# Optimization experiments

Hardware: AMD Instinct MI355X
Metric: run time of the kernel (lower is better)

Reference implementation:

```python
import jax, jax.numpy as jnp
import numpy as np

HIDDEN = 2560
NUM_HEADS = 80
HEAD_DIM = 64
STATE = 128
N_GROUPS = 1
CONV_K = 4
CHUNK = 256
INTER = 2 * HIDDEN                       # 5120 = NUM_HEADS * HEAD_DIM
CONV_DIM = INTER + 2 * N_GROUPS * STATE  # 5376
PROJ = INTER + CONV_DIM + NUM_HEADS      # 10576
EPS = 1e-5
DT_MIN, DT_MAX = 0.0, 100.0


def segment_sum(x):
    # x: (..., T) -> (..., T, T); out[i, j] = sum_{j < k <= i} x[k], -inf above diag
    T = x.shape[-1]
    xe = jnp.broadcast_to(x[..., :, None], x.shape + (T,))  # [i, j] = x[i]
    mask_lo = jnp.tril(jnp.ones((T, T), dtype=bool), -1)
    seg = jnp.cumsum(jnp.where(mask_lo, xe, 0.0), axis=-2)
    mask = jnp.tril(jnp.ones((T, T), dtype=bool), 0)
    return jnp.where(mask, seg, -jnp.inf)


def setup_inputs() -> dict:
    key = jax.random.key(0)
    k0, k1, k2, k3 = jax.random.split(key, 4)
    x = jax.random.normal(k0, (2, 2048, HIDDEN), jnp.float32)
    in_proj_w = jax.random.normal(k1, (PROJ, HIDDEN), jnp.float32) * (HIDDEN ** -0.5)
    conv1d_w = jax.random.normal(k2, (CONV_DIM, CONV_K), jnp.float32) * (CONV_K ** -0.5)
    conv1d_b = jnp.zeros((CONV_DIM,), jnp.float32)
    A_log = jnp.log(jnp.arange(1, NUM_HEADS + 1, dtype=jnp.float32))
    D = jnp.ones((NUM_HEADS,), jnp.float32)
    dt_bias = jnp.ones((NUM_HEADS,), jnp.float32)
    norm_weight = jnp.ones((INTER,), jnp.float32)
    out_proj_w = jax.random.normal(k3, (HIDDEN, INTER), jnp.float32) * (INTER ** -0.5)
    return dict(input_states=x, in_proj_w=in_proj_w, conv1d_w=conv1d_w,
                conv1d_b=conv1d_b, A_log=A_log, D=D, dt_bias=dt_bias,
                norm_weight=norm_weight, out_proj_w=out_proj_w)


def _mamba2_forward(input_states, in_proj_w, conv1d_w, conv1d_b, A_log, D,
                    dt_bias, norm_weight, out_proj_w):
    b, s, _ = input_states.shape
    proj = input_states @ in_proj_w.T                       # (b, s, PROJ)
    gate, hs, dt = jnp.split(proj, [INTER, INTER + CONV_DIM], axis=-1)

    # causal depthwise conv1d + SiLU
    xT = jnp.transpose(hs, (0, 2, 1))                       # (b, conv_dim, s)
    xT = jnp.pad(xT, ((0, 0), (0, 0), (CONV_K - 1, 0)))
    conv = jax.lax.conv_general_dilated(
        xT, conv1d_w[:, None, :], (1,), 'VALID',
        feature_group_count=CONV_DIM, dimension_numbers=('NCH', 'OIH', 'NCH'))
    hs = jax.nn.silu(jnp.transpose(conv + conv1d_b[None, :, None], (0, 2, 1)))

    hs, B, C = jnp.split(hs, [INTER, INTER + N_GROUPS * STATE], axis=-1)
    A = -jnp.exp(A_log)                                     # (h,)
    dt = jnp.clip(jax.nn.softplus(dt + dt_bias), DT_MIN, DT_MAX)  # (b, s, h)

    X = hs.reshape(b, s, NUM_HEADS, HEAD_DIM)
    rep = NUM_HEADS // N_GROUPS
    B = jnp.repeat(B.reshape(b, s, N_GROUPS, STATE), rep, axis=2)
    C = jnp.repeat(C.reshape(b, s, N_GROUPS, STATE), rep, axis=2)

    pad = (-s) % CHUNK
    D_res = D[None, None, :, None] * jnp.pad(X, ((0, 0), (0, pad), (0, 0), (0, 0)))
    Xd = X * dt[..., None]                                  # discretized input
    dA = A[None, None, :] * dt                              # (b, s, h)

    def chunk(t):
        t = jnp.pad(t, [(0, 0), (0, pad)] + [(0, 0)] * (t.ndim - 2))
        return t.reshape(t.shape[0], -1, CHUNK, *t.shape[2:])

    Xc, Bc, Cc = chunk(Xd), chunk(B), chunk(C)              # (b, c, l, h, ...)
    Ac = jnp.transpose(chunk(dA), (0, 3, 1, 2))             # (b, h, c, l)
    A_cum = jnp.cumsum(Ac, axis=-1)

    # 1. intra-chunk (diagonal block) outputs
    L = jnp.exp(segment_sum(Ac))                            # (b, h, c, l, l)
    G = jnp.einsum('bclhn,bcshn->bhcls', Cc, Bc)
    Y_diag = jnp.einsum('bhcls,bcshp->bclhp', G * L, Xc)

    # 2. per-chunk final states
    decay_states = jnp.exp(A_cum[..., -1:] - A_cum)         # (b, h, c, l)
    states = jnp.einsum('bclhn,bhcl,bclhp->bchpn', Bc, decay_states, Xc)

    # 3. inter-chunk recurrence
    A_last = A_cum[..., -1]                                 # (b, h, c)
    decay_chunk = jnp.exp(segment_sum(jnp.pad(A_last, ((0, 0), (0, 0), (1, 0)))))
    states = jnp.concatenate([jnp.zeros_like(states[:, :1]), states], axis=1)
    new_states = jnp.einsum('bhzc,bchpn->bzhpn', decay_chunk, states)
    states = new_states[:, :-1]                             # (b, c, h, p, n)

    # 4. state -> output conversion
    Y_off = jnp.einsum('bclhn,bchpn,bhcl->bclhp', Cc, states, jnp.exp(A_cum))

    y = (Y_diag + Y_off).reshape(b, -1, NUM_HEADS, HEAD_DIM) + D_res
    y = y[:, :s].reshape(b, s, INTER)

    # gated RMSNorm
    y = y * jax.nn.silu(gate)
    var = jnp.mean(y * y, axis=-1, keepdims=True)
    y = y * jax.lax.rsqrt(var + EPS) * norm_weight
    return y @ out_proj_w.T


def reference(input_states, in_proj_w, conv1d_w, conv1d_b, A_log, D, dt_bias,
              norm_weight, out_proj_w):
    return _mamba2_forward(input_states, in_proj_w, conv1d_w, conv1d_b, A_log,
                           D, dt_bias, norm_weight, out_proj_w)
```

## Files before the change

kernel.cpp:

```cpp
#include <hip/hip_runtime.h>
#include <hip/hip_bf16.h>
#include <math.h>

#define HIDDEN   2560
#define NUM_HEADS 80
#define HEAD_DIM 64
#define STATE    128
#define CONV_K   4
#define CHUNK    256
#define INTER    (2*HIDDEN)
#define CONV_DIM (INTER + 2*STATE)
#define PROJ     (INTER + CONV_DIM + NUM_HEADS)
#define PROJ_PAD 10240
#define NBC      336
#define NBCP     384
#define EPS      1e-5f

#define BATCH 2
#define SEQ   2048
#define TOK   (BATCH*SEQ)
#define NC    (SEQ/CHUNK)
#define KSPL2 8
#define KCH2  (HIDDEN/KSPL2)

#define RED_BLOCKS 1536
#define CXT_BLOCKS 5120
#define CBC_BLOCKS 4096
#define CUM_BLOCKS 1280
#define W2_BLOCKS  12800
#define ST_BLOCKS  1280
#define GK_BLOCKS  576

typedef __attribute__((ext_vector_type(8))) short bf16x8;
typedef __attribute__((ext_vector_type(4))) float f32x4;
typedef unsigned short us;

#define MFMA16(a,b,c) __builtin_amdgcn_mfma_f32_16x16x32_bf16((a),(b),(c),0,0,0)

__device__ __forceinline__ us f2bf(float f){
    union{float f;unsigned u;}v; v.f=f;
    unsigned r = v.u + 0x7fffu + ((v.u>>16)&1u);
    return (us)(r>>16);
}
__device__ __forceinline__ float bf2f(us s){
    union{unsigned u;float f;}v; v.u = ((unsigned)s)<<16; return v.f;
}
__device__ __forceinline__ void unpack8(uint4 u, float* e){
    e[0]=bf2f((us)(u.x&0xffff)); e[1]=bf2f((us)(u.x>>16));
    e[2]=bf2f((us)(u.y&0xffff)); e[3]=bf2f((us)(u.y>>16));
    e[4]=bf2f((us)(u.z&0xffff)); e[5]=bf2f((us)(u.z>>16));
    e[6]=bf2f((us)(u.w&0xffff)); e[7]=bf2f((us)(u.w>>16));
}
__device__ __forceinline__ void gld16(const void* g, void* l){
    __builtin_amdgcn_global_load_lds((const __attribute__((address_space(1))) void*)g,
                                     (__attribute__((address_space(3))) void*)l, 16, 0, 0);
}

template<bool BF16OUT>
__global__ __launch_bounds__(256) void gemm_bf16(const us* __restrict__ A, int lda,
                                                 const us* __restrict__ B, int ldb,
                                                 void* __restrict__ Cv, int ldc, int K) {
    __shared__ us As[128][64];
    __shared__ us Bs[128][64];
    int tid = threadIdx.x;
    int lane = tid & 63, wid = tid >> 6;
    int wr = wid >> 1, wc = wid & 1;

    int bm, bn;
    if ((gridDim.y & 7) == 0) {
        int bid   = blockIdx.y * gridDim.x + blockIdx.x;
        int xcd   = bid & 7;
        int local = bid >> 3;
        int mrows = gridDim.y >> 3;
        bm = (xcd * mrows + (local % mrows)) * 128;
        bn = (local / mrows) * 128;
    } else {
        bm = blockIdx.y * 128;
        bn = blockIdx.x * 128;
    }

    f32x4 acc[4][4];
    #pragma unroll
    for (int i=0;i<4;i++)
        #pragma unroll
        for (int j=0;j<4;j++) acc[i][j] = (f32x4){0.f,0.f,0.f,0.f};

    int srow_off = lane >> 3;
    int sslot    = lane & 7;

    for (int k0 = 0; k0 < K; k0 += 64) {
        #pragma unroll
        for (int q=0;q<4;q++){
            int brow = (wid*4+q)*8;
            int row  = brow + srow_off;
            int sl   = sslot ^ (row & 7);
            gld16(A + (size_t)(bm + row)*lda + k0 + sl*8, &As[brow][0]);
            gld16(B + (size_t)(bn + row)*ldb + k0 + sl*8, &Bs[brow][0]);
        }
        __syncthreads();
        #pragma unroll
        for (int kk=0; kk<64; kk+=32){
            bf16x8 a[4], b[4];
            #pragma unroll
            for (int i=0;i<4;i++){
                int row = wr*64 + i*16 + (lane&15);
                int slot = ((kk>>3) + (lane>>4)) ^ (row & 7);
                a[i] = *(const bf16x8*)&As[row][slot*8];
            }
            #pragma unroll
            for (int j=0;j<4;j++){
                int row = wc*64 + j*16 + (lane&15);
                int slot = ((kk>>3) + (lane>>4)) ^ (row & 7);
                b[j] = *(const bf16x8*)&Bs[row][slot*8];
            }
            #pragma unroll
            for (int i=0;i<4;i++)
                #pragma unroll
                for (int j=0;j<4;j++)
                    acc[i][j] = MFMA16(a[i], b[j], acc[i][j]);
        }
        __syncthreads();
    }
    #pragma unroll
    for (int i=0;i<4;i++){
        int row0 = bm + wr*64 + i*16 + (lane>>4)*4;
        #pragma unroll
        for (int j=0;j<4;j++){
            int col = bn + wc*64 + j*16 + (lane&15);
            #pragma unroll
            for (int r=0;r<4;r++){
                if (BF16OUT)
                    ((us*)Cv)[(size_t)(row0+r)*ldc + col] = f2bf(acc[i][j][r]);
                else
                    ((float*)Cv)[(size_t)(row0+r)*ldc + col] = acc[i][j][r];
            }
        }
    }
}

__global__ __launch_bounds__(256) void bc_splitk_mfma(const us* __restrict__ xhi,
                                                      const us* __restrict__ xlo,
                                                      const us* __restrict__ whi,
                                                      const us* __restrict__ wlo,
                                                      float* __restrict__ Cpart) {
    __shared__ us As[128][64];
    __shared__ us Bs[128][64];
    int tid = threadIdx.x;
    int lane = tid & 63, wid = tid >> 6;
    int wr = wid >> 1, wc = wid & 1;
    int bn = blockIdx.x * 128, bm = blockIdx.y * 128, z = blockIdx.z;

    f32x4 acc[4][4];
    #pragma unroll
    for (int i=0;i<4;i++)
        #pragma unroll
        for (int j=0;j<4;j++) acc[i][j] = (f32x4){0.f,0.f,0.f,0.f};

    int srow_off = lane >> 3;
    int sslot    = lane & 7;

    for (int term = 0; term < 3; ++term){
        const us* A = (term==2) ? xlo : xhi;
        const us* B = (term==0) ? wlo : whi;
        for (int k0 = z*KCH2; k0 < z*KCH2 + KCH2; k0 += 64) {
            #pragma unroll
            for (int q=0;q<4;q++){
                int brow = (wid*4+q)*8;
                int row  = brow + srow_off;
                int sl   = sslot ^ (row & 7);
                gld16(A + (size_t)(bm + row)*HIDDEN + k0 + sl*8, &As[brow][0]);
                gld16(B + (size_t)(bn + row)*HIDDEN + k0 + sl*8, &Bs[brow][0]);
            }
            __syncthreads();
            #pragma unroll
            for (int kk=0; kk<64; kk+=32){
                bf16x8 a[4], b[4];
                #pragma unroll
                for (int i=0;i<4;i++){
                    int row = wr*64 + i*16 + (lane&15);
                    int slot = ((kk>>3) + (lane>>4)) ^ (row & 7);
                    a[i] = *(const bf16x8*)&As[row][slot*8];
                }
                #pragma unroll
                for (int j=0;j<4;j++){
                    int row = wc*64 + j*16 + (lane&15);
                    int slot = ((kk>>3) + (lane>>4)) ^ (row & 7);
                    b[j] = *(const bf16x8*)&Bs[row][slot*8];
                }
                #pragma unroll
                for (int i=0;i<4;i++)
                    #pragma unroll
                    for (int j=0;j<4;j++)
                        acc[i][j] = MFMA16(a[i], b[j], acc[i][j]);
            }
            __syncthreads();
        }
    }
    float* Cz = Cpart + (size_t)z*TOK*NBCP;
    #pragma unroll
    for (int i=0;i<4;i++){
        int row0 = bm + wr*64 + i*16 + (lane>>4)*4;
        #pragma unroll
        for (int j=0;j<4;j++){
            int col = bn + wc*64 + j*16 + (lane&15);
            #pragma unroll
            for (int r=0;r<4;r++)
                Cz[(size_t)(row0+r)*NBCP + col] = acc[i][j][r];
        }
    }
}

#define N4A ((size_t)TOK*HIDDEN/4)
#define N4B ((size_t)PROJ_PAD*HIDDEN/4)
#define N4C ((size_t)NBCP*HIDDEN/4)
__global__ __launch_bounds__(256) void prep_kernel(const float* __restrict__ x,
                                                   const float* __restrict__ in_w,
                                                   us* __restrict__ xhi,
                                                   us* __restrict__ xlo,
                                                   us* __restrict__ w1b,
                                                   us* __restrict__ wbc_hi,
                                                   us* __restrict__ wbc_lo) {
    size_t gid = (size_t)blockIdx.x*256 + threadIdx.x;
    if (gid < N4A) {
        size_t i = gid*4;
        float4 v = *(const float4*)(x + i);
        float e[4] = {v.x, v.y, v.z, v.w};
        ushort4 h, l;
        us* hp = (us*)&h;
        us* lp = (us*)&l;
        #pragma unroll
        for (int u=0;u<4;u++){
            us hv = f2bf(e[u]);
            hp[u] = hv;
            lp[u] = f2bf(e[u] - bf2f(hv));
        }
        *(ushort4*)(xhi + i) = h;
        *(ushort4*)(xlo + i) = l;
    } else if (gid < N4A + N4B) {
        size_t i = (gid - N4A)*4;
        float4 v = *(const float4*)(in_w + i);
        ushort4 o;
        o.x=f2bf(v.x); o.y=f2bf(v.y); o.z=f2bf(v.z); o.w=f2bf(v.w);
        *(ushort4*)(w1b + i) = o;
    } else {
        size_t j = gid - N4A - N4B;
        size_t i = j*4;
        int row = (int)(i / HIDDEN);
        int kk  = (int)(i % HIDDEN);
        ushort4 h, l;
        h.x=h.y=h.z=h.w=0; l.x=l.y=l.z=l.w=0;
        if (row < NBC){
            float4 v = *(const float4*)(in_w + (size_t)(2*INTER + row)*HIDDEN + kk);
            float e[4] = {v.x, v.y, v.z, v.w};
            us* hp = (us*)&h;
            us* lp = (us*)&l;
            #pragma unroll
            for (int u=0;u<4;u++){
                us hv = f2bf(e[u]);
                hp[u] = hv;
                lp[u] = f2bf(e[u] - bf2f(hv));
            }
        }
        *(ushort4*)(wbc_hi + i) = h;
        *(ushort4*)(wbc_lo + i) = l;
    }
}

__global__ __launch_bounds__(256) void mega_red_convxt(const float* __restrict__ part,
                                                       const float* __restrict__ dt_bias,
                                                       const us* __restrict__ projb,
                                                       const float* __restrict__ cw,
                                                       const float* __restrict__ cb,
                                                       float* __restrict__ outBC,
                                                       float* __restrict__ dtbuf,
                                                       us* __restrict__ XT) {
    __shared__ us raw[68][66];
    int bid = blockIdx.x;
    int tid = threadIdx.x;
    if (bid < RED_BLOCKS) {
        size_t i4 = (size_t)bid*256 + tid;
        size_t i = i4*4;
        float4 s = *(const float4*)(part + i);
        #pragma unroll
        for (int z=1; z<KSPL2; z++){
            float4 v = *(const float4*)(part + (size_t)z*TOK*NBCP + i);
            s.x += v.x; s.y += v.y; s.z += v.z; s.w += v.w;
        }
        int col = (int)(i % NBCP);
        int t   = (int)(i / NBCP);
        if (col < 256) {
            *(float4*)(outBC + (size_t)t*NBC + col) = s;
        } else if (col < NBC) {
            int h = col - 256;
            float e[4] = {s.x, s.y, s.z, s.w};
            #pragma unroll
            for (int u=0;u<4;u++){
                float xv = e[u] + dt_bias[h+u];
                float sp = (xv > 20.f) ? xv : log1pf(expf(xv));
                e[u] = fminf(fmaxf(sp, 0.f), 100.f);
            }
            float4 o; o.x=e[0]; o.y=e[1]; o.z=e[2]; o.w=e[3];
            *(float4*)(dtbuf + (size_t)t*NUM_HEADS + h) = o;
        }
    } else {
        int b3 = bid - RED_BLOCKS;
        int bx = b3 & 63, by = b3 >> 6;
        int t0 = bx * 64, d0 = by * 64;
        int b  = t0 / SEQ;
        int s0 = t0 % SEQ;
        for (int f = tid; f < 67*8; f += 256){
            int r = f >> 3, g = f & 7;
            int sp = s0 - 3 + r;
            uint4 v;
            if (sp >= 0) v = *(const uint4*)(projb + ((size_t)(b*SEQ+sp))*PROJ_PAD + INTER + d0 + g*8);
            else { v.x=0u; v.y=0u; v.z=0u; v.w=0u; }
            unsigned int* dst = (unsigned int*)&raw[r][g*8];
            dst[0]=v.x; dst[1]=v.y; dst[2]=v.z; dst[3]=v.w;
        }
        __syncthreads();
        int t = tid & 63, dg = tid >> 6;
        #pragma unroll
        for (int dd = 0; dd < 16; dd++){
            int d = dg*16 + dd;
            float acc = cb[d0+d];
            #pragma unroll
            for (int j=0;j<CONV_K;j++)
                acc += cw[(d0+d)*CONV_K+j] * bf2f(raw[t+j][d]);
            float val = acc/(1.f+expf(-acc));
            XT[((size_t)(b*INTER + d0 + d))*SEQ + s0 + t] = f2bf(val);
        }
    }
}

__global__ __launch_bounds__(256) void mega_convbc_cum_w2(const float* __restrict__ projBC,
                                                          const float* __restrict__ cw,
                                                          const float* __restrict__ cb,
                                                          const float* __restrict__ dtbuf,
                                                          const float* __restrict__ A_log,
                                                          const float* __restrict__ out_w,
                                                          float* __restrict__ xBC_BC,
                                                          us* __restrict__ BT,
                                                          us* __restrict__ Cb,
                                                          float* __restrict__ A_cum,
                                                          us* __restrict__ w2b) {
    __shared__ float buf[CHUNK];
    int bid = blockIdx.x;
    int tid = threadIdx.x;
    if (bid < CBC_BLOCKS) {
        int idx = bid*256 + tid;
        int d = idx & 255;
        int t = idx >> 8;
        int b = t / SEQ, sl = t % SEQ;
        int dc = INTER + d;
        float acc = cb[dc];
        #pragma unroll
        for (int j=0;j<CONV_K;j++){
            int sp = sl - (CONV_K-1) + j;
            if (sp >= 0)
                acc += cw[dc*CONV_K+j] * projBC[((size_t)(b*SEQ+sp))*NBC + d];
        }
        float val = acc / (1.f + expf(-acc));
        xBC_BC[(size_t)t*256 + d] = val;
        if (d < 128)
            BT[((size_t)(b*128 + d))*SEQ + sl] = f2bf(val);
        else
            Cb[(size_t)t*128 + (d-128)] = f2bf(val);
    } else if (bid < CBC_BLOCKS + CUM_BLOCKS) {
        int b4 = bid - CBC_BLOCKS;
        int c = b4 & 7, h = (b4 >> 3) % 80, b = b4 / 640;
        int l = tid;
        float A = -expf(A_log[h]);
        float v = A * dtbuf[(size_t)(b*SEQ + c*CHUNK + l)*NUM_HEADS + h];
        buf[l] = v;
        __syncthreads();
        for (int off=1; off<CHUNK; off<<=1){
            float t2 = (l>=off) ? buf[l-off] : 0.f;
            __syncthreads();
            buf[l] += t2;
            __syncthreads();
        }
        A_cum[((size_t)b*NUM_HEADS + h)*SEQ + c*CHUNK + l] = buf[l];
    } else {
        size_t i4 = (size_t)(bid - CBC_BLOCKS - CUM_BLOCKS)*256 + tid;
        size_t i = i4*4;
        float4 v = *(const float4*)(out_w + i);
        ushort4 o; o.x=f2bf(v.x); o.y=f2bf(v.y); o.z=f2bf(v.z); o.w=f2bf(v.w);
        *(ushort4*)(w2b + i) = o;
    }
}

__global__ __launch_bounds__(256) void mega_states_g(const us* __restrict__ XT,
                                                     const us* __restrict__ BT,
                                                     const float* __restrict__ dtbuf,
                                                     const float* __restrict__ A_cum,
                                                     const float* __restrict__ xBC_BC,
                                                     us* __restrict__ statesT,
                                                     us* __restrict__ G) {
    __shared__ __align__(16) char SH[33792];
    int bid = blockIdx.x;
    int tid = threadIdx.x;
    if (bid < ST_BLOCKS) {
        int c = bid & 7, h = (bid >> 3) % 80, b = bid / 640;
        us (*Asx)[64] = (us(*)[64])SH;
        us (*Bs)[64]  = (us(*)[64])(SH + 8192);
        float* wl     = (float*)(SH + 24576);
        int lane = tid & 63, wid = tid >> 6;
        {
            const float* ac = A_cum + ((size_t)(b*NUM_HEADS+h))*SEQ + c*CHUNK;
            float Alast = ac[CHUNK-1];
            wl[tid] = expf(Alast - ac[tid]) * dtbuf[((size_t)(b*SEQ + c*CHUNK + tid))*NUM_HEADS + h];
        }
        __syncthreads();
        f32x4 acc[4][2];
        #pragma unroll
        for (int i=0;i<4;i++)
            #pragma unroll
            for (int j=0;j<2;j++) acc[i][j] = (f32x4){0.f,0.f,0.f,0.f};

        for (int kc = 0; kc < 4; kc++){
            int lbase = kc*64;
            #pragma unroll
            for (int q=0;q<4;q++){
                int brow = (wid*4+q)*8;
                int row  = brow + (lane>>3);
                int sl   = (lane&7) ^ (row & 7);
                gld16(BT + ((size_t)(b*128 + row))*SEQ + c*CHUNK + lbase + sl*8, &Bs[brow][0]);
            }
            #pragma unroll
            for (int it=0; it<2; it++){
                int f = tid + it*256;
                int r = f >> 3, g = f & 7;
                uint4 v = *(const uint4*)(XT + ((size_t)(b*INTER + h*HEAD_DIM + r))*SEQ + c*CHUNK + lbase + g*8);
                float e[8]; unpack8(v, e);
                us o[8];
                #pragma unroll
                for (int u=0;u<8;u++) o[u] = f2bf(e[u] * wl[lbase + g*8 + u]);
                int slot = g ^ (r & 7);
                *(ushort4*)&Asx[r][slot*8]   = *(ushort4*)&o[0];
                *(ushort4*)&Asx[r][slot*8+4] = *(ushort4*)&o[4];
            }
            __syncthreads();
            #pragma unroll
            for (int kk=0; kk<64; kk+=32){
                bf16x8 a[4], bb[2];
                #pragma unroll
                for (int i=0;i<4;i++){
                    int row = i*16 + (lane&15);
                    int slot = ((kk>>3)+(lane>>4)) ^ (row&7);
                    a[i] = *(const bf16x8*)&Asx[row][slot*8];
                }
                #pragma unroll
                for (int j=0;j<2;j++){
                    int row = wid*32 + j*16 + (lane&15);
                    int slot = ((kk>>3)+(lane>>4)) ^ (row&7);
                    bb[j] = *(const bf16x8*)&Bs[row][slot*8];
                }
                #pragma unroll
                for (int i=0;i<4;i++)
                    #pragma unroll
                    for (int j=0;j<2;j++)
                        acc[i][j] = MFMA16(a[i], bb[j], acc[i][j]);
            }
            __syncthreads();
        }
        size_t sb = ((size_t)((b*NC + c)*NUM_HEADS + h))*(HEAD_DIM*STATE);
        #pragma unroll
        for (int i=0;i<4;i++){
            #pragma unroll
            for (int j=0;j<2;j++){
                int n = wid*32 + j*16 + (lane&15);
                int p0 = i*16 + (lane>>4)*4;
                #pragma unroll
                for (int r=0;r<4;r++)
                    statesT[sb + (size_t)(p0+r)*128 + n] = f2bf(acc[i][j][r]);
            }
        }
    } else {
        int b5 = bid - ST_BLOCKS;
        int c = b5 & 7, p = (b5 >> 3) % 36, b = b5 / 288;
        int lt = 0, a0 = 0;
        while (a0 + lt + 1 <= p) { a0 += lt + 1; lt++; }
        int st = p - a0;
        int l0 = lt*32, s0 = st*32;
        float (*Cs)[132] = (float(*)[132])SH;
        float (*Bs2)[132] = (float(*)[132])(SH + 16896);
        int ty = tid >> 4, tx = tid & 15;
        float acc[2][2];
        acc[0][0]=0.f; acc[0][1]=0.f; acc[1][0]=0.f; acc[1][1]=0.f;

        size_t rowC = ((size_t)(b*SEQ + c*CHUNK + l0))*256 + 128;
        size_t rowB = ((size_t)(b*SEQ + c*CHUNK + s0))*256;
        #pragma unroll
        for (int it=0; it<4; it++){
            int f = tid + it*256;
            int r = f >> 5, c4 = f & 31;
            *(float4*)&Cs[r][c4*4]  = *(const float4*)(xBC_BC + rowC + (size_t)r*256 + c4*4);
            *(float4*)&Bs2[r][c4*4] = *(const float4*)(xBC_BC + rowB + (size_t)r*256 + c4*4);
        }
        __syncthreads();
        #pragma unroll 8
        for (int k=0;k<128;k++){
            float a0v = Cs[ty*2][k],   a1v = Cs[ty*2+1][k];
            float b0v = Bs2[tx*2][k],  b1v = Bs2[tx*2+1][k];
            acc[0][0] += a0v*b0v; acc[0][1] += a0v*b1v;
            acc[1][0] += a1v*b0v; acc[1][1] += a1v*b1v;
        }
        size_t Gb = ((size_t)(b*NC + c)) << 16;
        #pragma unroll
        for (int i=0;i<2;i++){
            ushort2 g2;
            g2.x = f2bf(acc[i][0]); g2.y = f2bf(acc[i][1]);
            *(ushort2*)(G + Gb + (size_t)(l0 + ty*2 + i)*256 + s0 + tx*2) = g2;
        }
    }
}

__global__ __launch_bounds__(256) void recur_kernel(const float* __restrict__ A_cum,
                                                    us* __restrict__ states) {
    int h = blockIdx.x, b = blockIdx.y, z = blockIdx.z;
    int tid = threadIdx.x;
    float Srun[8];
    #pragma unroll
    for (int i=0;i<8;i++) Srun[i]=0.f;
    const float* acum = A_cum + ((size_t)b*NUM_HEADS + h)*SEQ;
    for (int c=0;c<NC;c++){
        float alast = acum[c*CHUNK + CHUNK-1];
        float dec = expf(alast);
        size_t base = ((size_t)((b*NC + c)*NUM_HEADS + h))*(HEAD_DIM*STATE);
        #pragma unroll
        for (int i=0;i<8;i++){
            size_t idx = base + (size_t)tid + (size_t)(z*8+i)*256;
            float raw = bf2f(states[idx]);
            states[idx] = f2bf(Srun[i]);
            Srun[i] = Srun[i]*dec + raw;
        }
    }
}

__global__ __launch_bounds__(256) void yscan_mfma(const us* __restrict__ G,
                                                  const us* __restrict__ Cb,
                                                  const us* __restrict__ XT,
                                                  const float* __restrict__ dtbuf,
                                                  const float* __restrict__ A_cum,
                                                  const us* __restrict__ statesT,
                                                  const float* __restrict__ Dvec,
                                                  us* __restrict__ projb) {
    int xb = blockIdx.x;
    int c = xb & 7, lt = xb >> 3;
    int h = blockIdx.y, b = blockIdx.z;
    int l0 = lt*64;
    __shared__ __align__(16) char pool[32768];
    us (*Cs)[128] = (us(*)[128])pool;
    us (*St)[128] = (us(*)[128])(pool + 16384);
    us (*Gw)[64]  = (us(*)[64])pool;
    us (*Xs)[64]  = (us(*)[64])(pool + 8192);
    float (*Ot)[68] = (float(*)[68])pool;
    __shared__ float ac[CHUNK], dts[CHUNK];
    int tid = threadIdx.x, lane = tid & 63, wid = tid >> 6;
    ac[tid]  = A_cum[((size_t)(b*NUM_HEADS + h))*SEQ + c*CHUNK + tid];
    dts[tid] = dtbuf[((size_t)(b*SEQ + c*CHUNK + tid))*NUM_HEADS + h];

    size_t stb = ((size_t)((b*NC + c)*NUM_HEADS + h))*(HEAD_DIM*STATE);
    #pragma unroll
    for (int q=0;q<4;q++){
        int brow = (wid*4+q)*4;
        int row  = brow + (lane>>4);
        int sl   = (lane&15) ^ (row & 7);
        gld16(Cb + ((size_t)(b*SEQ + c*CHUNK + l0 + row))*128 + sl*8, &Cs[brow][0]);
        gld16(statesT + stb + (size_t)row*128 + sl*8, &St[brow][0]);
    }
    __syncthreads();

    f32x4 acc1[4];
    #pragma unroll
    for (int j=0;j<4;j++) acc1[j] = (f32x4){0.f,0.f,0.f,0.f};
    #pragma unroll
    for (int kk=0; kk<128; kk+=32){
        int arow = wid*16 + (lane&15);
        int aslot = ((kk>>3)+(lane>>4)) ^ (arow&7);
        bf16x8 a = *(const bf16x8*)&Cs[arow][aslot*8];
        #pragma unroll
        for (int j=0;j<4;j++){
            int brow = j*16 + (lane&15);
            int bslot = ((kk>>3)+(lane>>4)) ^ (brow&7);
            bf16x8 bb = *(const bf16x8*)&St[brow][bslot*8];
            acc1[j] = MFMA16(a, bb, acc1[j]);
        }
    }
    float el[4];
    #pragma unroll
    for (int r=0;r<4;r++) el[r] = expf(ac[l0 + wid*16 + (lane>>4)*4 + r]);
    float master[4][4];
    #pragma unroll
    for (int j=0;j<4;j++)
        #pragma unroll
        for (int r=0;r<4;r++) master[j][r] = acc1[j][r]*el[r];
    __syncthreads();

    size_t Gb = ((size_t)(b*NC + c)) << 16;
    f32x4 acc2[4];
    #pragma unroll
    for (int j=0;j<4;j++) acc2[j] = (f32x4){0.f,0.f,0.f,0.f};
    for (int st=0; st<=lt; st++){
        int s0 = st*64;
        #pragma unroll
        for (int it=0; it<2; it++){
            int f = tid + it*256;
            int r = f >> 3, g = f & 7;
            uint4 v = *(const uint4*)(G + Gb + (size_t)(l0 + r)*256 + s0 + g*8);
            float e[8]; unpack8(v, e);
            float acl = ac[l0 + r];
            us o[8];
            #pragma unroll
            for (int u=0;u<8;u++){
                int s = s0 + g*8 + u;
                float w = (s <= l0 + r) ? expf(acl - ac[s])*dts[s] : 0.f;
                o[u] = f2bf(e[u]*w);
            }
            int slot = g ^ (r&7);
            *(ushort4*)&Gw[r][slot*8]   = *(ushort4*)&o[0];
            *(ushort4*)&Gw[r][slot*8+4] = *(ushort4*)&o[4];
        }
        #pragma unroll
        for (int q=0;q<2;q++){
            int brow = (wid*2+q)*8;
            int row  = brow + (lane>>3);
            int sl   = (lane&7) ^ (row&7);
            gld16(XT + ((size_t)(b*INTER + h*HEAD_DIM + row))*SEQ + c*CHUNK + s0 + sl*8,
                  &Xs[brow][0]);
        }
        __syncthreads();
        #pragma unroll
        for (int kk=0; kk<64; kk+=32){
            int arow = wid*16 + (lane&15);
            int aslot = ((kk>>3)+(lane>>4)) ^ (arow&7);
            bf16x8 a = *(const bf16x8*)&Gw[arow][aslot*8];
            #pragma unroll
            for (int j=0;j<4;j++){
                int brow = j*16 + (lane&15);
                int bslot = ((kk>>3)+(lane>>4)) ^ (brow&7);
                bf16x8 bb = *(const bf16x8*)&Xs[brow][bslot*8];
                acc2[j] = MFMA16(a, bb, acc2[j]);
            }
        }
        if (st < lt) __syncthreads();
    }

    float Dh = Dvec[h];
    #pragma unroll
    for (int j=0;j<4;j++){
        int p = j*16 + (lane&15);
        #pragma unroll
        for (int r=0;r<4;r++){
            int sl_ = wid*16 + (lane>>4)*4 + r;
            int slot = (sl_>>3) ^ (p&7);
            float xv = bf2f(Xs[p][slot*8 + (sl_&7)]);
            master[j][r] += acc2[j][r] + Dh*xv;
        }
    }
    __syncthreads();

    #pragma unroll
    for (int j=0;j<4;j++){
        int p = j*16 + (lane&15);
        #pragma unroll
        for (int r=0;r<4;r++)
            Ot[wid*16 + (lane>>4)*4 + r][p] = master[j][r];
    }
    __syncthreads();
    #pragma unroll
    for (int it=0; it<4; it++){
        int f = tid + it*256;
        int r = f >> 4, c4 = f & 15;
        ushort4 o;
        o.x = f2bf(Ot[r][c4*4+0]); o.y = f2bf(Ot[r][c4*4+1]);
        o.z = f2bf(Ot[r][c4*4+2]); o.w = f2bf(Ot[r][c4*4+3]);
        *(ushort4*)(projb + ((size_t)(b*SEQ + c*CHUNK + l0 + r))*PROJ_PAD + INTER + h*HEAD_DIM + c4*4) = o;
    }
}

__global__ __launch_bounds__(256) void gate_norm_kernel(const us* __restrict__ projb,
                                                        const float* __restrict__ normw,
                                                        us* __restrict__ yb) {
    int t = blockIdx.x;
    int tid = threadIdx.x;
    const us* row = projb + (size_t)t*PROJ_PAD;
    __shared__ float red[4];
    float vals[20];
    float ss = 0.f;
    #pragma unroll
    for (int i=0;i<5;i++){
        int j = (tid + i*256)*4;
        ushort4 g4 = *(const ushort4*)(row + j);
        ushort4 y4 = *(const ushort4*)(row + INTER + j);
        #pragma unroll
        for (int u=0;u<4;u++){
            float g = bf2f(((const us*)&g4)[u]);
            float y = bf2f(((const us*)&y4)[u]);
            float gv = g / (1.f + expf(-g));
            float v = y * gv;
            vals[i*4+u] = v;
            ss += v*v;
        }
    }
    #pragma unroll
    for (int off=32; off; off>>=1) ss += __shfl_xor(ss, off);
    if ((tid&63)==0) red[tid>>6] = ss;
    __syncthreads();
    float tot = red[0]+red[1]+red[2]+red[3];
    float inv = rsqrtf(tot/(float)INTER + EPS);
    #pragma unroll
    for (int i=0;i<5;i++){
        int j = (tid + i*256)*4;
        ushort4 o;
        o.x = f2bf(vals[i*4+0] * inv * normw[j+0]);
        o.y = f2bf(vals[i*4+1] * inv * normw[j+1]);
        o.z = f2bf(vals[i*4+2] * inv * normw[j+2]);
        o.w = f2bf(vals[i*4+3] * inv * normw[j+3]);
        *(ushort4*)(yb + (size_t)t*INTER + j) = o;
    }
}

extern "C" void kernel_launch(void* const* d_in, const int* in_sizes, int n_in,
                              void* d_out, int out_size, void* d_ws, size_t ws_size,
                              hipStream_t stream) {
    const float* x        = (const float*)d_in[0];
    const float* in_w     = (const float*)d_in[1];
    const float* conv_w   = (const float*)d_in[2];
    const float* conv_b   = (const float*)d_in[3];
    const float* A_log    = (const float*)d_in[4];
    const float* Dvec     = (const float*)d_in[5];
    const float* dt_bias  = (const float*)d_in[6];
    const float* norm_w   = (const float*)d_in[7];
    const float* out_w    = (const float*)d_in[8];
    float* out = (float*)d_out;
    (void)ws_size; (void)n_in; (void)in_sizes; (void)out_size;

    const size_t PROJB   = (size_t)TOK*PROJ_PAD*2;
    const size_t PROJBCB = (size_t)TOK*NBC*4;
    const size_t XTB     = (size_t)TOK*INTER*2;
    const size_t XBCBCB  = (size_t)TOK*256*4;
    const size_t BTB     = (size_t)BATCH*128*SEQ*2;
    const size_t CBB     = (size_t)TOK*128*2;
    const size_t GBYTES  = (size_t)BATCH*NC*CHUNK*CHUNK*2;
    const size_t DTB     = (size_t)TOK*NUM_HEADS*4;
    const size_t ACUMB   = DTB;
    const size_t STB     = (size_t)BATCH*NC*NUM_HEADS*HEAD_DIM*STATE*2;
    const size_t XHB   = (size_t)TOK*HIDDEN*2;
    const size_t WBCB  = (size_t)NBCP*HIDDEN*2;
    const size_t YBB   = (size_t)TOK*INTER*2;

    char* base = (char*)d_ws;
    size_t off = 0;
    us* projb  = (us*)(base + off); off += PROJB;
    float* projBC = (float*)(base + off); off += PROJBCB;
    us* XTp    = (us*)(base + off); off += XTB;
    float* xBC_BC = (float*)(base + off); off += XBCBCB;
    us* BTp    = (us*)(base + off); off += BTB;
    us* Cbp    = (us*)(base + off); off += CBB;
    us* Gp     = (us*)(base + off); off += GBYTES;
    float* dtbuf = (float*)(base + off); off += DTB;
    float* A_cum = (float*)(base + off); off += ACUMB;
    us* statesT = (us*)(base + off); off += STB;
    char*  T   = base + off;
    us* xhi    = (us*)T;
    us* xlo    = (us*)(T + XHB);
    us* wbc_hi = (us*)(T + 2*XHB);
    us* wbc_lo = (us*)(T + 2*XHB + WBCB);
    us* w1b    = (us*)(T + 2*XHB + 2*WBCB);
    float* bcpart = (float*)w1b;
    us* yb     = (us*)T;
    us* w2b    = (us*)(T + YBB);

    {
        unsigned total_blocks = (unsigned)((N4A + N4B + N4C) / 256);
        prep_kernel<<<total_blocks, 256, 0, stream>>>(x, in_w, xhi, xlo, w1b, wbc_hi, wbc_lo);
    }
    gemm_bf16<true><<<dim3(PROJ_PAD/128, TOK/128), 256, 0, stream>>>(xhi, HIDDEN, w1b, HIDDEN,
                                                                     projb, PROJ_PAD, HIDDEN);
    bc_splitk_mfma<<<dim3(NBCP/128, TOK/128, KSPL2), 256, 0, stream>>>(xhi, xlo, wbc_hi, wbc_lo, bcpart);
    mega_red_convxt<<<RED_BLOCKS + CXT_BLOCKS, 256, 0, stream>>>(bcpart, dt_bias, projb,
                                                                 conv_w, conv_b,
                                                                 projBC, dtbuf, XTp);
    mega_convbc_cum_w2<<<CBC_BLOCKS + CUM_BLOCKS + W2_BLOCKS, 256, 0, stream>>>(
        projBC, conv_w, conv_b, dtbuf, A_log, out_w, xBC_BC, BTp, Cbp, A_cum, w2b);
    mega_states_g<<<ST_BLOCKS + GK_BLOCKS, 256, 0, stream>>>(XTp, BTp, dtbuf, A_cum, xBC_BC,
                                                             statesT, Gp);
    recur_kernel<<<dim3(NUM_HEADS, BATCH, 4), 256, 0, stream>>>(A_cum, statesT);
    yscan_mfma<<<dim3(NC*4, NUM_HEADS, BATCH), 256, 0, stream>>>(Gp, Cbp, XTp, dtbuf, A_cum,
                                                                 statesT, Dvec, projb);
    gate_norm_kernel<<<TOK, 256, 0, stream>>>(projb, norm_w, yb);
    gemm_bf16<false><<<dim3(HIDDEN/128, TOK/128), 256, 0, stream>>>(yb, INTER, w2b, INTER,
                                                                    out, HIDDEN, INTER);
}
```

Baseline: 705.1 us.

## Replace input projection GEMM with 256x256 tile, 8-wave phased pipelined kernel

Swaps the 128x128-tile input projection GEMM for a new 512-thread kernel that computes 256x256 output tiles. It double-buffers K-halves in LDS through direct global-to-LDS loads and interleaves prefetch stages with MFMA sub-phases under explicit waitcnt and barrier control, raising s_setprio around the MFMA bursts. The larger tile raises arithmetic intensity and the phased schedule aims to hide load latency. In exchange it uses more registers per thread and gives a smaller grid (40x16 blocks), which may reduce occupancy and leave tail imbalance.

```diff
diff --git a/kernel.cpp b/kernel.cpp
--- a/kernel.cpp
+++ b/kernel.cpp
@@ -54,6 +54,99 @@
 __device__ __forceinline__ void gld16(const void* g, void* l){
     __builtin_amdgcn_global_load_lds((const __attribute__((address_space(1))) void*)g,
                                      (__attribute__((address_space(3))) void*)l, 16, 0, 0);
+}
+
+__global__ __launch_bounds__(512) void gemm1_8ph(const us* __restrict__ A,
+                                                 const us* __restrict__ B,
+                                                 us* __restrict__ C, int ldc) {
+    __shared__ us LA[2][2][256][32];
+    __shared__ us LB[2][2][256][32];
+    int tid = threadIdx.x, lane = tid & 63, wid = tid >> 6;
+    int wm = wid >> 2, wn = wid & 3;
+
+    int bid   = blockIdx.y * gridDim.x + blockIdx.x;
+    int xcd   = bid & 7;
+    int local = bid >> 3;
+    int mrows = gridDim.y >> 3;
+    int bm = (xcd * mrows + (local % mrows)) * 256;
+    int bn = (local / mrows) * 256;
+
+    f32x4 acc[8][4];
+    #pragma unroll
+    for (int i=0;i<8;i++)
+        #pragma unroll
+        for (int j=0;j<4;j++) acc[i][j] = (f32x4){0.f,0.f,0.f,0.f};
+
+    const int NT = HIDDEN/64;
+
+    #define STGA(TT,KH) { _Pragma("unroll")                                        \
+        for (int q=0;q<2;q++){                                                     \
+            int brow=(wid*2+q)*16; int row=brow+(lane>>2);                         \
+            int sl=(lane&3)^((row>>1)&3);                                          \
+            gld16(A + (size_t)(bm+row)*HIDDEN + (TT)*64 + (KH)*32 + sl*8,          \
+                  &LA[(TT)&1][KH][brow][0]); } }
+    #define STGB(TT,KH) { _Pragma("unroll")                                        \
+        for (int q=0;q<2;q++){                                                     \
+            int brow=(wid*2+q)*16; int row=brow+(lane>>2);                         \
+            int sl=(lane&3)^((row>>1)&3);                                          \
+            gld16(B + (size_t)(bn+row)*HIDDEN + (TT)*64 + (KH)*32 + sl*8,          \
+                  &LB[(TT)&1][KH][brow][0]); } }
+
+    STGA(0,0); STGB(0,0); STGA(0,1); STGB(0,1); STGA(1,0); STGB(1,0);
+    asm volatile("s_waitcnt vmcnt(8)" ::: "memory");
+    asm volatile("s_barrier" ::: "memory");
+
+    for (int t = 0; t < NT; ++t) {
+        int par = t & 1;
+        #pragma unroll
+        for (int sub = 0; sub < 4; ++sub) {
+            const int kh = sub >> 1, mg = sub & 1;
+            bf16x8 afr[4], bfr[4];
+            #pragma unroll
+            for (int mi=0;mi<4;mi++){
+                int row = wm*128 + (mg*4+mi)*16 + (lane&15);
+                int sl  = (lane>>4) ^ ((row>>1)&3);
+                afr[mi] = *(const bf16x8*)&LA[par][kh][row][sl*8];
+            }
+            #pragma unroll
+            for (int nj=0;nj<4;nj++){
+                int row = wn*64 + nj*16 + (lane&15);
+                int sl  = (lane>>4) ^ ((row>>1)&3);
+                bfr[nj] = *(const bf16x8*)&LB[par][kh][row][sl*8];
+            }
+            if      (sub==0) { if (t+1<NT) STGA(t+1,1); }
+            else if (sub==1) { if (t+1<NT) STGB(t+1,1); }
+            else if (sub==2) { if (t+2<NT) STGA(t+2,0); }
+            else             { if (t+2<NT) STGB(t+2,0); }
+            asm volatile("s_barrier" ::: "memory");
+            __builtin_amdgcn_s_setprio(1);
+            #pragma unroll
+            for (int mi=0;mi<4;mi++)
+                #pragma unroll
+                for (int nj=0;nj<4;nj++)
+                    acc[mg*4+mi][nj] = MFMA16(afr[mi], bfr[nj], acc[mg*4+mi][nj]);
+            __builtin_amdgcn_s_setprio(0);
+            if (sub==1 || sub==3) {
+                if (t < NT-2) asm volatile("s_waitcnt vmcnt(8)" ::: "memory");
+                else          asm volatile("s_waitcnt vmcnt(0)" ::: "memory");
+            }
+            asm volatile("s_barrier" ::: "memory");
+        }
+    }
+    #undef STGA
+    #undef STGB
+
+    #pragma unroll
+    for (int i=0;i<8;i++){
+        int row0 = bm + wm*128 + i*16 + (lane>>4)*4;
+        #pragma unroll
+        for (int j=0;j<4;j++){
+            int col = bn + wn*64 + j*16 + (lane&15);
+            #pragma unroll
+            for (int r=0;r<4;r++)
+                C[(size_t)(row0+r)*ldc + col] = f2bf(acc[i][j][r]);
+        }
+    }
 }
 
 template<bool BF16OUT>
@@ -776,8 +869,7 @@
         unsigned total_blocks = (unsigned)((N4A + N4B + N4C) / 256);
         prep_kernel<<<total_blocks, 256, 0, stream>>>(x, in_w, xhi, xlo, w1b, wbc_hi, wbc_lo);
     }
-    gemm_bf16<true><<<dim3(PROJ_PAD/128, TOK/128), 256, 0, stream>>>(xhi, HIDDEN, w1b, HIDDEN,
-                                                                     projb, PROJ_PAD, HIDDEN);
+    gemm1_8ph<<<dim3(PROJ_PAD/256, TOK/256), 512, 0, stream>>>(xhi, w1b, projb, PROJ_PAD);
     bc_splitk_mfma<<<dim3(NBCP/128, TOK/128, KSPL2), 256, 0, stream>>>(xhi, xlo, wbc_hi, wbc_lo, bcpart);
     mega_red_convxt<<<RED_BLOCKS + CXT_BLOCKS, 256, 0, stream>>>(bcpart, dt_bias, projb,
                                                                  conv_w, conv_b,
```

Result: slower. 732.7 us (+3.9%).
